# Kernel tuning notes

Measured on AMD Instinct MI355X. Metric: run time of the kernel, lower is better.

The kernel has to match this reference:

```python
import jax, jax.numpy as jnp
import numpy as np

B, C, D, H, W = 2, 128, 32, 64, 64  # ch_in=128, shurink=0 -> Cs = ch_out = C
Cs = C


def setup_inputs() -> dict:
    key = jax.random.key(0)
    ks = jax.random.split(key, 9)
    std = 1.0 / np.sqrt(C).astype(np.float32)
    x = jax.random.normal(ks[0], (B, C, D, H, W), jnp.float32)
    Wk = jax.random.normal(ks[1], (Cs, C), jnp.float32) * std
    bk = jax.random.normal(ks[2], (Cs,), jnp.float32) * std
    Wq = jax.random.normal(ks[3], (Cs, C), jnp.float32) * std
    bq = jax.random.normal(ks[4], (Cs,), jnp.float32) * std
    Wv = jax.random.normal(ks[5], (Cs, C), jnp.float32) * std
    bv = jax.random.normal(ks[6], (Cs,), jnp.float32) * std
    Wo = jax.random.normal(ks[7], (C, Cs), jnp.float32) * (1.0 / np.sqrt(Cs).astype(np.float32))
    bo = jax.random.normal(ks[8], (C,), jnp.float32) * std
    return {"x": x, "Wk": Wk, "bk": bk, "Wq": Wq, "bq": bq, "Wv": Wv, "bv": bv, "Wo": Wo, "bo": bo}


def reference(x, Wk, bk, Wq, bq, Wv, bv, Wo, bo):
    # 1x1x1 Conv3d == per-voxel linear over channels
    def proj(Wt, bt):
        return jnp.einsum('bcdhw,oc->bodhw', x, Wt) + bt[None, :, None, None, None]

    K = proj(Wk, bk)  # [B,Cs,D,H,W]
    Q = proj(Wq, bq)
    V = proj(Wv, bv)

    scale = 1.0 / jnp.sqrt(jnp.asarray(Cs, x.dtype))
    # per-pixel depth attention: scores[b,h,w,i,j] = sum_c K[b,c,i,h,w] * Q[b,c,j,h,w]
    scores = jnp.einsum('bcihw,bcjhw->bhwij', K, Q) * scale
    # torch softmax dim=1 on [N,D,D] == key-position axis i (axis=-2 here)
    A = jax.nn.softmax(scores, axis=-2)
    # a[b,c,j,h,w] = sum_i V[b,c,i,h,w] * A[b,h,w,i,j]  (== bmm(V, A))
    a = jnp.einsum('bcihw,bhwij->bcjhw', V, A)
    out = jnp.einsum('bcjhw,oc->bojhw', a, Wo) + bo[None, :, None, None, None]
    return x + out  # atten_factor = 1
```

## Files before the change

kernel.cpp:

```cpp
#include <hip/hip_runtime.h>

typedef _Float16 f16x8 __attribute__((ext_vector_type(8)));
typedef _Float16 f16x4 __attribute__((ext_vector_type(4)));
typedef float    f32x4 __attribute__((ext_vector_type(4)));

#define MFMA(a,b,c) __builtin_amdgcn_mfma_f32_16x16x32_f16((a),(b),(c),0,0,0)


__global__ __launch_bounds__(128) void prep_kernel(
    const float* __restrict__ Wk, const float* __restrict__ bk,
    const float* __restrict__ Wq, const float* __restrict__ bq,
    const float* __restrict__ Wv, const float* __restrict__ bv,
    const float* __restrict__ Wo, const float* __restrict__ bo,
    _Float16* __restrict__ wh, float* __restrict__ bf) {
  __shared__ float shK[128], shO[128];
  const int o = blockIdx.x;
  const int c = threadIdx.x;
  const float scale = 0.08838834764831844f;
  shK[c] = Wk[c*128 + o];
  shO[c] = Wo[o*128 + c];
  __syncthreads();
  float aM = 0.f, aV = 0.f, tK = 0.f, bV = 0.f;
  for (int m = 0; m < 128; ++m) {
    aM += shK[m] * Wq[m*128 + c];
    aV += shO[m] * Wv[m*128 + c];
    tK += shK[m] * bq[m];
    bV += shO[m] * bv[m];
  }
  wh[o*128 + c]         = (_Float16)(aM * scale);
  wh[16384 + o*128 + c] = (_Float16)aV;
  if (c == 0) { bf[o] = tK * scale; bf[128 + o] = bV + bo[o]; }
}

__global__ __launch_bounds__(256) void transpose_kernel(
    const float* __restrict__ x, _Float16* __restrict__ Xg) {
  __shared__ _Float16 Lt[64 * 130];
  const int bid = blockIdx.x;
  const int h = bid & 63, d = (bid >> 6) & 31, b = bid >> 11;
  const int tid = threadIdx.x;
  const size_t rbase = (size_t)b*16777216u + (size_t)d*4096 + h*64;
#pragma unroll
  for (int i = 0; i < 8; ++i) {
    const int chunk = tid + i*256;
    const int c = chunk >> 4, wq = chunk & 15;
    const f32x4 v = *(const f32x4*)(x + rbase + (size_t)c*131072 + wq*4);
    Lt[(wq*4+0)*130 + c] = (_Float16)v[0];
    Lt[(wq*4+1)*130 + c] = (_Float16)v[1];
    Lt[(wq*4+2)*130 + c] = (_Float16)v[2];
    Lt[(wq*4+3)*130 + c] = (_Float16)v[3];
  }
  __syncthreads();
  const int gbase = b*1024 + h*16;
#pragma unroll
  for (int i = 0; i < 4; ++i) {
    const int idx = tid + i*256;
    const int w = idx >> 4, ck = (idx & 15) * 8;
    const int wg = w >> 2, p = w & 3;
    const f16x8 v = *(const f16x8*)(Lt + w*130 + ck);
    *(f16x8*)(Xg + (size_t)(gbase + wg)*16384 + (d*4 + p)*128 + ck) = v;
  }
}

__device__ __forceinline__ f16x4 cvt4(f32x4 v, f32x4 b) {
  f16x4 r;
  r[0] = (_Float16)(v[0] + b[0]); r[1] = (_Float16)(v[1] + b[1]);
  r[2] = (_Float16)(v[2] + b[2]); r[3] = (_Float16)(v[3] + b[3]);
  return r;
}
__device__ __forceinline__ f16x4 cvt4z(f32x4 v) {
  f16x4 r;
  r[0] = (_Float16)v[0]; r[1] = (_Float16)v[1];
  r[2] = (_Float16)v[2]; r[3] = (_Float16)v[3];
  return r;
}

__device__ __forceinline__ int xsw(int row, int col ) {
  return ((row << 8) | (col << 1)) ^ (((row ^ (row >> 2)) & 7) << 4);
}

__global__ __launch_bounds__(1024, 8) void attn_kernel(
    const _Float16* __restrict__ Xg, const _Float16* __restrict__ wh,
    const float* __restrict__ bfp, float* __restrict__ out) {
  __shared__ __align__(16) char lds[75776];
  char* XtB = lds;
  char* YtB = lds + 32768;
  _Float16* At = (_Float16*)(lds + 65536);

  const int tid  = threadIdx.x;
  const int lane = tid & 63;
  const int wv   = tid >> 6;
  const int quad = lane >> 4;
  const int l15  = lane & 15;

  const int bid = blockIdx.x;
  const int g = (bid & ~31) | ((bid & 7) << 2) | ((bid >> 3) & 3);
  const int b   = g >> 10;
  const int rem = g & 1023;
  const int h   = rem >> 4;
  const int wg  = rem & 15;
  const size_t pbase = (size_t)b * 16777216u + (size_t)(h*64 + wg*4);
  const f32x4 zz = {0.f, 0.f, 0.f, 0.f};

  const int mi = wv & 7, ni = wv >> 3;
  f16x8 wm[4];
#pragma unroll
  for (int kk = 0; kk < 4; ++kk)
    wm[kk] = *(const f16x8*)(wh + (mi*16 + l15)*128 + kk*32 + quad*8);
  const f32x4 t4 = *(const f32x4*)(bfp + mi*16 + quad*4);

  {
    const _Float16* src = Xg + (size_t)g * 16384;
#pragma unroll
    for (int i = 0; i < 2; ++i) {
      const int idx = tid + i*1024;
      const int row = idx >> 4, ck = (idx & 15) * 8;
      const f16x8 v = *(const f16x8*)(src + row*128 + ck);
      *(f16x8*)(XtB + xsw(row, ck)) = v;
    }
  }
  __syncthreads();

  {
    f32x4 aY[4] = {zz, zz, zz, zz};
#pragma unroll
    for (int kk = 0; kk < 4; ++kk) {
      const int co = kk*32 + quad*8;
#pragma unroll
      for (int nt = 0; nt < 4; ++nt) {
        const f16x8 bfv = *(const f16x8*)(XtB + xsw(ni*64 + nt*16 + l15, co));
        aY[nt] = MFMA(wm[kk], bfv, aY[nt]);
      }
    }
#pragma unroll
    for (int nt = 0; nt < 4; ++nt)
      *(f16x4*)(YtB + xsw(ni*64 + nt*16 + l15, mi*16 + quad*4)) = cvt4(aY[nt], t4);
  }
  __syncthreads();

  if (wv < 4) {
    const int p = wv;
    f32x4 aS[2][2] = {{zz, zz}, {zz, zz}};
#pragma unroll
    for (int kk = 0; kk < 4; ++kk) {
      const int co = kk*32 + quad*8;
      f16x8 ak[2], by[2];
#pragma unroll
      for (int t = 0; t < 2; ++t) {
        ak[t] = *(const f16x8*)(XtB + xsw((t*16 + l15)*4 + p, co));
        by[t] = *(const f16x8*)(YtB + xsw((t*16 + l15)*4 + p, co));
      }
#pragma unroll
      for (int ti = 0; ti < 2; ++ti)
#pragma unroll
        for (int tj = 0; tj < 2; ++tj)
          aS[ti][tj] = MFMA(ak[ti], by[tj], aS[ti][tj]);
    }
#pragma unroll
    for (int tj = 0; tj < 2; ++tj) {
      float mx = aS[0][tj][0];
#pragma unroll
      for (int r = 1; r < 4; ++r) mx = fmaxf(mx, aS[0][tj][r]);
#pragma unroll
      for (int r = 0; r < 4; ++r) mx = fmaxf(mx, aS[1][tj][r]);
      mx = fmaxf(mx, __shfl_xor(mx, 16));
      mx = fmaxf(mx, __shfl_xor(mx, 32));
      float e[2][4];
      float den = 0.f;
#pragma unroll
      for (int ti = 0; ti < 2; ++ti)
#pragma unroll
        for (int r = 0; r < 4; ++r) { e[ti][r] = __expf(aS[ti][tj][r] - mx); den += e[ti][r]; }
      den += __shfl_xor(den, 16);
      den += __shfl_xor(den, 32);
      const float rr = 1.0f / den;
#pragma unroll
      for (int ti = 0; ti < 2; ++ti) {
        f16x4 av;
#pragma unroll
        for (int r = 0; r < 4; ++r) av[r] = (_Float16)(e[ti][r] * rr);
        *(f16x4*)(At + (p*32 + tj*16 + l15)*40 + ti*16 + quad*4) = av;
      }
    }
  }
  __syncthreads();

  f16x8 wp[4];
  {
#pragma unroll
    for (int kk = 0; kk < 4; ++kk)
      wp[kk] = *(const f16x8*)(wh + 16384 + ((wv & 7)*16 + l15)*128 + kk*32 + quad*8);
    const int p = wv & 3, mg = wv >> 2;
    f16x8 bA[2];
#pragma unroll
    for (int tj = 0; tj < 2; ++tj)
      bA[tj] = *(const f16x8*)(At + (p*32 + tj*16 + l15)*40 + quad*8);
#pragma unroll
    for (int t2 = 0; t2 < 2; ++t2) {
      const int ms = mg*2 + t2;
      f16x8 ax;
#pragma unroll
      for (int jj = 0; jj < 8; ++jj)
        ax[jj] = *(const _Float16*)(XtB + xsw((quad*8 + jj)*4 + p, ms*16 + l15));
#pragma unroll
      for (int tj = 0; tj < 2; ++tj) {
        const f32x4 aU = MFMA(ax, bA[tj], zz);
        *(f16x4*)(YtB + xsw((tj*16 + l15)*4 + p, ms*16 + quad*4)) = cvt4z(aU);
      }
    }
  }
  __syncthreads();

  {
    const int oi = wv & 7, mg6 = wv >> 3;
    f32x4 acc[4] = {zz, zz, zz, zz};
#pragma unroll
    for (int kk = 0; kk < 4; ++kk) {
      const int co = kk*32 + quad*8;
#pragma unroll
      for (int mt = 0; mt < 4; ++mt) {
        const f16x8 av = *(const f16x8*)(YtB + xsw((mg6*4 + mt)*16 + l15, co));
        acc[mt] = MFMA(av, wp[kk], acc[mt]);
      }
    }
    const int o = oi*16 + l15;
    const float bb = bfp[128 + o];
    float* outp = out + pbase + (size_t)o*131072;
#pragma unroll
    for (int mt = 0; mt < 4; ++mt) {
      const int colb = (mg6*4 + mt)*16 + quad*4;
      const int d = colb >> 2;
      f32x4 v;
#pragma unroll
      for (int r = 0; r < 4; ++r)
        v[r] = acc[mt][r] + bb +
               (float)*(const _Float16*)(XtB + xsw(colb + r, o));
      *(f32x4*)(outp + (size_t)d*4096) = v;
    }
  }
}

extern "C" void kernel_launch(void* const* d_in, const int* in_sizes, int n_in,
                              void* d_out, int out_size, void* d_ws, size_t ws_size,
                              hipStream_t stream) {
  const float* x  = (const float*)d_in[0];
  const float* Wk = (const float*)d_in[1];
  const float* bk = (const float*)d_in[2];
  const float* Wq = (const float*)d_in[3];
  const float* bq = (const float*)d_in[4];
  const float* Wv = (const float*)d_in[5];
  const float* bv = (const float*)d_in[6];
  const float* Wo = (const float*)d_in[7];
  const float* bo = (const float*)d_in[8];
  float* out = (float*)d_out;
  _Float16* wh = (_Float16*)d_ws;
  float* bf = (float*)((char*)d_ws + 65536);
  _Float16* Xg = (_Float16*)((char*)d_ws + 131072);

  prep_kernel<<<dim3(128), dim3(128), 0, stream>>>(Wk, bk, Wq, bq, Wv, bv, Wo, bo, wh, bf);
  transpose_kernel<<<dim3(4096), dim3(256), 0, stream>>>(x, Xg);
  attn_kernel<<<dim3(2048), dim3(1024), 0, stream>>>(Xg, wh, bf, out);
}
```

Measured before the change: 370.4 us.

## Make attention kernel persistent with prefetch and MFMA-based residual add

The attention kernel now runs 512 blocks that each loop over four tiles, prefetching the next tile's fp16 input into registers while the current tile finishes the output projection. The residual add is folded into the output MFMA by multiplying the x tile against an identity-pattern fragment, replacing scalar LDS reads. The transpose kernel is reworked so each thread loads four channels and writes packed f16x4 to a padded LDS tile, replacing scalar half stores. Trade-offs: fewer blocks means less latency hiding across blocks, plus an extra MFMA pass and an extra barrier per iteration.

```diff
diff --git a/kernel.cpp b/kernel.cpp
--- a/kernel.cpp
+++ b/kernel.cpp
@@ -34,20 +34,26 @@
 
 __global__ __launch_bounds__(256) void transpose_kernel(
     const float* __restrict__ x, _Float16* __restrict__ Xg) {
-  __shared__ _Float16 Lt[64 * 130];
+  __shared__ _Float16 Lt[64 * 132];
   const int bid = blockIdx.x;
   const int h = bid & 63, d = (bid >> 6) & 31, b = bid >> 11;
   const int tid = threadIdx.x;
+  const int wq = tid & 15, cr = tid >> 4;
   const size_t rbase = (size_t)b*16777216u + (size_t)d*4096 + h*64;
 #pragma unroll
-  for (int i = 0; i < 8; ++i) {
-    const int chunk = tid + i*256;
-    const int c = chunk >> 4, wq = chunk & 15;
-    const f32x4 v = *(const f32x4*)(x + rbase + (size_t)c*131072 + wq*4);
-    Lt[(wq*4+0)*130 + c] = (_Float16)v[0];
-    Lt[(wq*4+1)*130 + c] = (_Float16)v[1];
-    Lt[(wq*4+2)*130 + c] = (_Float16)v[2];
-    Lt[(wq*4+3)*130 + c] = (_Float16)v[3];
+  for (int pass = 0; pass < 2; ++pass) {
+    const int base_c = pass*64 + cr*4;
+    f32x4 v[4];
+#pragma unroll
+    for (int r = 0; r < 4; ++r)
+      v[r] = *(const f32x4*)(x + rbase + (size_t)(base_c + r)*131072 + wq*4);
+#pragma unroll
+    for (int p = 0; p < 4; ++p) {
+      f16x4 t;
+#pragma unroll
+      for (int r = 0; r < 4; ++r) t[r] = (_Float16)v[r][p];
+      *(f16x4*)(Lt + (wq*4 + p)*132 + base_c) = t;
+    }
   }
   __syncthreads();
   const int gbase = b*1024 + h*16;
@@ -55,9 +61,8 @@
   for (int i = 0; i < 4; ++i) {
     const int idx = tid + i*256;
     const int w = idx >> 4, ck = (idx & 15) * 8;
-    const int wg = w >> 2, p = w & 3;
-    const f16x8 v = *(const f16x8*)(Lt + w*130 + ck);
-    *(f16x8*)(Xg + (size_t)(gbase + wg)*16384 + (d*4 + p)*128 + ck) = v;
+    const f16x8 v = *(const f16x8*)(Lt + w*132 + ck);
+    *(f16x8*)(Xg + (size_t)(gbase + (w>>2))*16384 + (d*4 + (w&3))*128 + ck) = v;
   }
 }
 
@@ -91,151 +96,181 @@
   const int wv   = tid >> 6;
   const int quad = lane >> 4;
   const int l15  = lane & 15;
-
-  const int bid = blockIdx.x;
-  const int g = (bid & ~31) | ((bid & 7) << 2) | ((bid >> 3) & 3);
-  const int b   = g >> 10;
-  const int rem = g & 1023;
-  const int h   = rem >> 4;
-  const int wg  = rem & 15;
-  const size_t pbase = (size_t)b * 16777216u + (size_t)(h*64 + wg*4);
+  const int bid  = blockIdx.x;
   const f32x4 zz = {0.f, 0.f, 0.f, 0.f};
 
   const int mi = wv & 7, ni = wv >> 3;
+  const int oi = wv & 7, mg6 = wv >> 3;
+  const int row1 = (tid + 0)    >> 4, ck1 = ((tid + 0)    & 15) * 8;
+  const int row2 = (tid + 1024) >> 4, ck2 = ((tid + 1024) & 15) * 8;
+
   f16x8 wm[4];
 #pragma unroll
   for (int kk = 0; kk < 4; ++kk)
     wm[kk] = *(const f16x8*)(wh + (mi*16 + l15)*128 + kk*32 + quad*8);
   const f32x4 t4 = *(const f32x4*)(bfp + mi*16 + quad*4);
-
+  const float bb = bfp[128 + oi*16 + l15];
+
+  const int ck0 = (oi >> 1) * 32;
+  union { f16x8 h; unsigned int u[4]; } wid;
   {
-    const _Float16* src = Xg + (size_t)g * 16384;
-#pragma unroll
-    for (int i = 0; i < 2; ++i) {
-      const int idx = tid + i*1024;
-      const int row = idx >> 4, ck = (idx & 15) * 8;
-      const f16x8 v = *(const f16x8*)(src + row*128 + ck);
-      *(f16x8*)(XtB + xsw(row, ck)) = v;
-    }
-  }
-  __syncthreads();
-
-  {
-    f32x4 aY[4] = {zz, zz, zz, zz};
-#pragma unroll
-    for (int kk = 0; kk < 4; ++kk) {
-      const int co = kk*32 + quad*8;
-#pragma unroll
-      for (int nt = 0; nt < 4; ++nt) {
-        const f16x8 bfv = *(const f16x8*)(XtB + xsw(ni*64 + nt*16 + l15, co));
-        aY[nt] = MFMA(wm[kk], bfv, aY[nt]);
-      }
-    }
-#pragma unroll
-    for (int nt = 0; nt < 4; ++nt)
-      *(f16x4*)(YtB + xsw(ni*64 + nt*16 + l15, mi*16 + quad*4)) = cvt4(aY[nt], t4);
-  }
-  __syncthreads();
-
-  if (wv < 4) {
-    const int p = wv;
-    f32x4 aS[2][2] = {{zz, zz}, {zz, zz}};
-#pragma unroll
-    for (int kk = 0; kk < 4; ++kk) {
-      const int co = kk*32 + quad*8;
-      f16x8 ak[2], by[2];
-#pragma unroll
-      for (int t = 0; t < 2; ++t) {
-        ak[t] = *(const f16x8*)(XtB + xsw((t*16 + l15)*4 + p, co));
-        by[t] = *(const f16x8*)(YtB + xsw((t*16 + l15)*4 + p, co));
-      }
-#pragma unroll
-      for (int ti = 0; ti < 2; ++ti)
-#pragma unroll
-        for (int tj = 0; tj < 2; ++tj)
-          aS[ti][tj] = MFMA(ak[ti], by[tj], aS[ti][tj]);
-    }
-#pragma unroll
-    for (int tj = 0; tj < 2; ++tj) {
-      float mx = aS[0][tj][0];
-#pragma unroll
-      for (int r = 1; r < 4; ++r) mx = fmaxf(mx, aS[0][tj][r]);
-#pragma unroll
-      for (int r = 0; r < 4; ++r) mx = fmaxf(mx, aS[1][tj][r]);
-      mx = fmaxf(mx, __shfl_xor(mx, 16));
-      mx = fmaxf(mx, __shfl_xor(mx, 32));
-      float e[2][4];
-      float den = 0.f;
-#pragma unroll
-      for (int ti = 0; ti < 2; ++ti)
-#pragma unroll
-        for (int r = 0; r < 4; ++r) { e[ti][r] = __expf(aS[ti][tj][r] - mx); den += e[ti][r]; }
-      den += __shfl_xor(den, 16);
-      den += __shfl_xor(den, 32);
-      const float rr = 1.0f / den;
-#pragma unroll
-      for (int ti = 0; ti < 2; ++ti) {
-        f16x4 av;
-#pragma unroll
-        for (int r = 0; r < 4; ++r) av[r] = (_Float16)(e[ti][r] * rr);
-        *(f16x4*)(At + (p*32 + tj*16 + l15)*40 + ti*16 + quad*4) = av;
-      }
-    }
-  }
-  __syncthreads();
-
-  f16x8 wp[4];
-  {
-#pragma unroll
-    for (int kk = 0; kk < 4; ++kk)
-      wp[kk] = *(const f16x8*)(wh + 16384 + ((wv & 7)*16 + l15)*128 + kk*32 + quad*8);
-    const int p = wv & 3, mg = wv >> 2;
-    f16x8 bA[2];
-#pragma unroll
-    for (int tj = 0; tj < 2; ++tj)
-      bA[tj] = *(const f16x8*)(At + (p*32 + tj*16 + l15)*40 + quad*8);
-#pragma unroll
-    for (int t2 = 0; t2 < 2; ++t2) {
-      const int ms = mg*2 + t2;
-      f16x8 ax;
-#pragma unroll
-      for (int jj = 0; jj < 8; ++jj)
-        ax[jj] = *(const _Float16*)(XtB + xsw((quad*8 + jj)*4 + p, ms*16 + l15));
+    const int t = (oi & 1)*16 + l15;
+    const unsigned int ones = 0x3C00u << ((t & 1) * 16);
+    const int hot = (quad == (t >> 3));
+    const int j0 = (t >> 1) & 3;
+    wid.u[0] = (hot && j0 == 0) ? ones : 0u;
+    wid.u[1] = (hot && j0 == 1) ? ones : 0u;
+    wid.u[2] = (hot && j0 == 2) ? ones : 0u;
+    wid.u[3] = (hot && j0 == 3) ? ones : 0u;
+  }
+
+  int orig = bid;
+  int g = (orig & ~31) | ((orig & 7) << 2) | ((orig >> 3) & 3);
+  f16x8 pf0 = *(const f16x8*)(Xg + (size_t)g*16384 + row1*128 + ck1);
+  f16x8 pf1 = *(const f16x8*)(Xg + (size_t)g*16384 + row2*128 + ck2);
+
+  for (int it = 0; it < 4; ++it) {
+    const int b   = g >> 10;
+    const int rem = g & 1023;
+    const size_t pbase = (size_t)b * 16777216u + (size_t)((rem >> 4)*64 + (rem & 15)*4);
+
+    *(f16x8*)(XtB + xsw(row1, ck1)) = pf0;
+    *(f16x8*)(XtB + xsw(row2, ck2)) = pf1;
+    __syncthreads();
+
+    {
+      f32x4 aY[4] = {zz, zz, zz, zz};
+#pragma unroll
+      for (int kk = 0; kk < 4; ++kk) {
+        const int co = kk*32 + quad*8;
+#pragma unroll
+        for (int nt = 0; nt < 4; ++nt) {
+          const f16x8 bfv = *(const f16x8*)(XtB + xsw(ni*64 + nt*16 + l15, co));
+          aY[nt] = MFMA(wm[kk], bfv, aY[nt]);
+        }
+      }
+#pragma unroll
+      for (int nt = 0; nt < 4; ++nt)
+        *(f16x4*)(YtB + xsw(ni*64 + nt*16 + l15, mi*16 + quad*4)) = cvt4(aY[nt], t4);
+    }
+    __syncthreads();
+
+    if (wv < 4) {
+      const int p = wv;
+      f32x4 aS[2][2] = {{zz, zz}, {zz, zz}};
+#pragma unroll
+      for (int kk = 0; kk < 4; ++kk) {
+        const int co = kk*32 + quad*8;
+        f16x8 ak[2], by[2];
+#pragma unroll
+        for (int t = 0; t < 2; ++t) {
+          ak[t] = *(const f16x8*)(XtB + xsw((t*16 + l15)*4 + p, co));
+          by[t] = *(const f16x8*)(YtB + xsw((t*16 + l15)*4 + p, co));
+        }
+#pragma unroll
+        for (int ti = 0; ti < 2; ++ti)
+#pragma unroll
+          for (int tj = 0; tj < 2; ++tj)
+            aS[ti][tj] = MFMA(ak[ti], by[tj], aS[ti][tj]);
+      }
 #pragma unroll
       for (int tj = 0; tj < 2; ++tj) {
-        const f32x4 aU = MFMA(ax, bA[tj], zz);
-        *(f16x4*)(YtB + xsw((tj*16 + l15)*4 + p, ms*16 + quad*4)) = cvt4z(aU);
-      }
-    }
-  }
-  __syncthreads();
-
-  {
-    const int oi = wv & 7, mg6 = wv >> 3;
-    f32x4 acc[4] = {zz, zz, zz, zz};
-#pragma unroll
-    for (int kk = 0; kk < 4; ++kk) {
-      const int co = kk*32 + quad*8;
+        float mx = aS[0][tj][0];
+#pragma unroll
+        for (int r = 1; r < 4; ++r) mx = fmaxf(mx, aS[0][tj][r]);
+#pragma unroll
+        for (int r = 0; r < 4; ++r) mx = fmaxf(mx, aS[1][tj][r]);
+        mx = fmaxf(mx, __shfl_xor(mx, 16));
+        mx = fmaxf(mx, __shfl_xor(mx, 32));
+        float e[2][4];
+        float den = 0.f;
+#pragma unroll
+        for (int ti = 0; ti < 2; ++ti)
+#pragma unroll
+          for (int r = 0; r < 4; ++r) { e[ti][r] = __expf(aS[ti][tj][r] - mx); den += e[ti][r]; }
+        den += __shfl_xor(den, 16);
+        den += __shfl_xor(den, 32);
+        const float rr = 1.0f / den;
+#pragma unroll
+        for (int ti = 0; ti < 2; ++ti) {
+          f16x4 av;
+#pragma unroll
+          for (int r = 0; r < 4; ++r) av[r] = (_Float16)(e[ti][r] * rr);
+          *(f16x4*)(At + (p*32 + tj*16 + l15)*40 + ti*16 + quad*4) = av;
+        }
+      }
+    }
+    __syncthreads();
+
+    {
+      f16x8 wp_[4];
+#pragma unroll
+      for (int kk = 0; kk < 4; ++kk)
+        wp_[kk] = *(const f16x8*)(wh + 16384 + (mi*16 + l15)*128 + kk*32 + quad*8);
+      (void)wp_[0];
+      const int p = wv & 3, mg = wv >> 2;
+      f16x8 bA[2];
+#pragma unroll
+      for (int tj = 0; tj < 2; ++tj)
+        bA[tj] = *(const f16x8*)(At + (p*32 + tj*16 + l15)*40 + quad*8);
+#pragma unroll
+      for (int t2 = 0; t2 < 2; ++t2) {
+        const int ms = mg*2 + t2;
+        f16x8 ax;
+#pragma unroll
+        for (int jj = 0; jj < 8; ++jj)
+          ax[jj] = *(const _Float16*)(XtB + xsw((quad*8 + jj)*4 + p, ms*16 + l15));
+#pragma unroll
+        for (int tj = 0; tj < 2; ++tj) {
+          const f32x4 aU = MFMA(ax, bA[tj], zz);
+          *(f16x4*)(YtB + xsw((tj*16 + l15)*4 + p, ms*16 + quad*4)) = cvt4z(aU);
+        }
+      }
+    }
+    __syncthreads();
+
+    if (it < 3) {
+      const int orign = orig + 512;
+      const int gn = (orign & ~31) | ((orign & 7) << 2) | ((orign >> 3) & 3);
+      pf0 = *(const f16x8*)(Xg + (size_t)gn*16384 + row1*128 + ck1);
+      pf1 = *(const f16x8*)(Xg + (size_t)gn*16384 + row2*128 + ck2);
+      orig = orign;
+      g = gn;
+    }
+
+    {
+      f16x8 wp[4];
+#pragma unroll
+      for (int kk = 0; kk < 4; ++kk)
+        wp[kk] = *(const f16x8*)(wh + 16384 + (oi*16 + l15)*128 + kk*32 + quad*8);
+      f32x4 acc[4] = {zz, zz, zz, zz};
+#pragma unroll
+      for (int kk = 0; kk < 4; ++kk) {
+        const int co = kk*32 + quad*8;
+#pragma unroll
+        for (int mt = 0; mt < 4; ++mt) {
+          const f16x8 av = *(const f16x8*)(YtB + xsw((mg6*4 + mt)*16 + l15, co));
+          acc[mt] = MFMA(av, wp[kk], acc[mt]);
+        }
+      }
 #pragma unroll
       for (int mt = 0; mt < 4; ++mt) {
-        const f16x8 av = *(const f16x8*)(YtB + xsw((mg6*4 + mt)*16 + l15, co));
-        acc[mt] = MFMA(av, wp[kk], acc[mt]);
-      }
-    }
-    const int o = oi*16 + l15;
-    const float bb = bfp[128 + o];
-    float* outp = out + pbase + (size_t)o*131072;
-#pragma unroll
-    for (int mt = 0; mt < 4; ++mt) {
-      const int colb = (mg6*4 + mt)*16 + quad*4;
-      const int d = colb >> 2;
-      f32x4 v;
-#pragma unroll
-      for (int r = 0; r < 4; ++r)
-        v[r] = acc[mt][r] + bb +
-               (float)*(const _Float16*)(XtB + xsw(colb + r, o));
-      *(f32x4*)(outp + (size_t)d*4096) = v;
-    }
+        const f16x8 axr = *(const f16x8*)(XtB + xsw((mg6*4 + mt)*16 + l15, ck0 + quad*8));
+        acc[mt] = MFMA(axr, wid.h, acc[mt]);
+      }
+      const int o = oi*16 + l15;
+      float* outp = out + pbase + (size_t)o*131072;
+#pragma unroll
+      for (int mt = 0; mt < 4; ++mt) {
+        const int colb = (mg6*4 + mt)*16 + quad*4;
+        const int d = colb >> 2;
+        f32x4 v;
+#pragma unroll
+        for (int r = 0; r < 4; ++r) v[r] = acc[mt][r] + bb;
+        *(f32x4*)(outp + (size_t)d*4096) = v;
+      }
+    }
+    __syncthreads();
   }
 }
 
@@ -258,5 +293,5 @@
 
   prep_kernel<<<dim3(128), dim3(128), 0, stream>>>(Wk, bk, Wq, bq, Wv, bv, Wo, bo, wh, bf);
   transpose_kernel<<<dim3(4096), dim3(256), 0, stream>>>(x, Xg);
-  attn_kernel<<<dim3(2048), dim3(1024), 0, stream>>>(Xg, wh, bf, out);
-}
+  attn_kernel<<<dim3(512), dim3(1024), 0, stream>>>(Xg, wh, bf, out);
+}
```

New measurement: 540.2 us. +45.8%, slower.
